# Optimization experiments

Hardware: AMD Instinct MI355X
Metric: run time of the kernel (lower is better)

The kernel has to match this reference:

```python
import jax, jax.numpy as jnp
import numpy as np

N = 20000      # num_atoms
C = 64         # num_features (channels)
I = 16         # num_irreps = (l_max+1)^2, l_max=3
K2, K1, K0 = 120, 8, 4  # CG basis sizes per correlation order


def setup_inputs() -> dict:
    key = jax.random.key(0)
    ks = jax.random.split(key, 7)
    return {
        "node_feats": jax.random.normal(ks[0], (N, C, I), jnp.float32),
        "U2": jax.random.normal(ks[1], (I, I, I, K2), jnp.float32),
        "U1": jax.random.normal(ks[2], (I, I, K1), jnp.float32),
        "U0": jax.random.normal(ks[3], (I, K0), jnp.float32),
        "w2": jax.random.normal(ks[4], (K2, C), jnp.float32),
        "w1": jax.random.normal(ks[5], (K1, C), jnp.float32),
        "w0": jax.random.normal(ks[6], (K0, C), jnp.float32),
    }


def reference(node_feats, U2, U1, U0, w2, w1, w0):
    # equation_main: '...ik,kc,bci -> bc...' with U2 [I,I,I,K2]
    # -> out [N, C, I, I]
    out = jnp.einsum('xyik,kc,nci->ncxy', U2, w2, node_feats)

    # corr = 1: weighting '...k,kc->c...' then contract 'bc...i,bci->bc...'
    c1 = jnp.einsum('xik,kc->cxi', U1, w1)          # [C, I, I]
    out = jnp.einsum('ncxi,nci->ncx', c1 + out, node_feats)  # [N, C, I]

    # corr = 0
    c0 = jnp.einsum('ik,kc->ci', U0, w0)            # [C, I]
    out = jnp.einsum('nci,nci->nc', c0 + out, node_feats)    # [N, C]
    return out
```

## Files before the change

kernel.cpp:

```cpp
#include <hip/hip_runtime.h>

#define NATOMS 20000
#define NCHAN  64
#define NIRR   16
#define K2 120
#define K1 8
#define K0 4

#define W1_BYTE_OFF 524288
#define W0_BYTE_OFF 557056

#define NT 10

typedef __attribute__((ext_vector_type(8))) short bf16x8;
typedef __attribute__((ext_vector_type(4))) float f32x4;
typedef __attribute__((ext_vector_type(4))) unsigned int u32x4;

__device__ inline short f2bf(float f) {
    union { float f; unsigned u; } v; v.f = f;
    unsigned r = v.u + 0x7FFF + ((v.u >> 16) & 1);
    return (short)(r >> 16);
}

__global__ __launch_bounds__(256) void precompute_kernel(
    const float* __restrict__ U2, const float* __restrict__ U1,
    const float* __restrict__ U0, const float* __restrict__ w2,
    const float* __restrict__ w1, const float* __restrict__ w0,
    void* __restrict__ wsv)
{
    short* W2bf = (short*)wsv;
    short* W1bf = (short*)((char*)wsv + W1_BYTE_OFF);
    float* W0f  = (float*)((char*)wsv + W0_BYTE_OFF);

    const int b = blockIdx.x;
    const int t = threadIdx.x;

    if (b < 256) {
        __shared__ __align__(16) float U2s[64][121];
        __shared__ __align__(16) float w2s[120][16];
        const int xyi0  = (b >> 2) * 64;
        const int cbase = (b & 3) * 16;

        for (int o = t; o < 64 * 120; o += 256) {
            int r = o / 120, k = o - r * 120;
            U2s[r][k] = U2[(size_t)xyi0 * 120 + o];
        }
        for (int o = t; o < 120 * 16; o += 256) {
            int k = o >> 4, cc = o & 15;
            w2s[k][cc] = w2[k * NCHAN + cbase + cc];
        }
        __syncthreads();

        const int r = t & 63;
        const int g = t >> 6;
        float acc0 = 0.f, acc1 = 0.f, acc2 = 0.f, acc3 = 0.f;
        #pragma unroll 8
        for (int k = 0; k < 120; ++k) {
            float u = U2s[r][k];
            float4 w = *(const float4*)&w2s[k][g * 4];
            acc0 += u * w.x; acc1 += u * w.y; acc2 += u * w.z; acc3 += u * w.w;
        }
        const int xyi = xyi0 + r;
        const int cA  = cbase + g * 4;
        W2bf[(size_t)(cA + 0) * 4096 + xyi] = f2bf(acc0);
        W2bf[(size_t)(cA + 1) * 4096 + xyi] = f2bf(acc1);
        W2bf[(size_t)(cA + 2) * 4096 + xyi] = f2bf(acc2);
        W2bf[(size_t)(cA + 3) * 4096 + xyi] = f2bf(acc3);
    } else {
        const int lb = b - 256;
        for (int o = t; o < 2048; o += 256) {
            int go = lb * 2048 + o;
            int c = go >> 8, xy = go & 255;
            const float* u = U1 + xy * K1;
            float acc = 0.f;
            #pragma unroll
            for (int k = 0; k < K1; ++k) acc += u[k] * w1[k * NCHAN + c];
            W1bf[c * 256 + xy] = f2bf(acc);
        }
        if (lb == 0) {
            for (int o = t; o < 1024; o += 256) {
                int c = o >> 4, x = o & 15;
                const float* u = U0 + x * K0;
                float acc = 0.f;
                #pragma unroll
                for (int k = 0; k < K0; ++k) acc += u[k] * w0[k * NCHAN + c];
                W0f[c * 16 + x] = acc;
            }
        }
    }
}

__device__ __forceinline__ void gload_lds16(const void* g, void* l) {
    __builtin_amdgcn_global_load_lds(
        (const __attribute__((address_space(1))) unsigned int*)g,
        (__attribute__((address_space(3))) unsigned int*)l, 16, 0, 0);
}

__device__ __forceinline__ float compute_tile(
    const bf16x8 (&aw)[16], float4 c0, int q,
    float4 va, float4 vb, float4 vc, float4 vd)
{
    float f0 = va.x, f1 = va.y, f2 = va.z, f3 = va.w;
    float f4 = vb.x, f5 = vb.y, f6 = vb.z, f7 = vb.w;
    float f8 = vc.x, f9 = vc.y, f10 = vc.z, f11 = vc.w;
    float f12 = vd.x, f13 = vd.y, f14 = vd.z, f15 = vd.w;

    unsigned pk0, pk1, pk2, pk3, pk4, pk5, pk6, pk7;
    asm("v_cvt_pk_bf16_f32 %0, %1, %2" : "=v"(pk0) : "v"(f0),  "v"(f1));
    asm("v_cvt_pk_bf16_f32 %0, %1, %2" : "=v"(pk1) : "v"(f2),  "v"(f3));
    asm("v_cvt_pk_bf16_f32 %0, %1, %2" : "=v"(pk2) : "v"(f4),  "v"(f5));
    asm("v_cvt_pk_bf16_f32 %0, %1, %2" : "=v"(pk3) : "v"(f6),  "v"(f7));
    asm("v_cvt_pk_bf16_f32 %0, %1, %2" : "=v"(pk4) : "v"(f8),  "v"(f9));
    asm("v_cvt_pk_bf16_f32 %0, %1, %2" : "=v"(pk5) : "v"(f10), "v"(f11));
    asm("v_cvt_pk_bf16_f32 %0, %1, %2" : "=v"(pk6) : "v"(f12), "v"(f13));
    asm("v_cvt_pk_bf16_f32 %0, %1, %2" : "=v"(pk7) : "v"(f14), "v"(f15));

    unsigned w0s = (q == 0) ? pk0 : (q == 1) ? pk4 : (q == 2) ? 0x00003f80u : 0u;
    unsigned w1s = (q == 0) ? pk1 : (q == 1) ? pk5 : 0u;
    unsigned w2s_ = (q == 0) ? pk2 : (q == 1) ? pk6 : 0u;
    unsigned w3s = (q == 0) ? pk3 : (q == 1) ? pk7 : 0u;
    u32x4 bu = {w0s, w1s, w2s_, w3s};
    bf16x8 bfr = __builtin_bit_cast(bf16x8, bu);

    const f32x4 z = {0.f, 0.f, 0.f, 0.f};
    f32x4 sy = z;
    f32x4 d0 = __builtin_amdgcn_mfma_f32_16x16x32_bf16(aw[0], bfr, z, 0, 0, 0);
    f32x4 d1 = __builtin_amdgcn_mfma_f32_16x16x32_bf16(aw[1], bfr, z, 0, 0, 0);
    f32x4 d2 = __builtin_amdgcn_mfma_f32_16x16x32_bf16(aw[2], bfr, z, 0, 0, 0);
    f32x4 d3 = __builtin_amdgcn_mfma_f32_16x16x32_bf16(aw[3], bfr, z, 0, 0, 0);
    sy += d0 * f0;  d0 = __builtin_amdgcn_mfma_f32_16x16x32_bf16(aw[4],  bfr, z, 0, 0, 0);
    sy += d1 * f1;  d1 = __builtin_amdgcn_mfma_f32_16x16x32_bf16(aw[5],  bfr, z, 0, 0, 0);
    sy += d2 * f2;  d2 = __builtin_amdgcn_mfma_f32_16x16x32_bf16(aw[6],  bfr, z, 0, 0, 0);
    sy += d3 * f3;  d3 = __builtin_amdgcn_mfma_f32_16x16x32_bf16(aw[7],  bfr, z, 0, 0, 0);
    sy += d0 * f4;  d0 = __builtin_amdgcn_mfma_f32_16x16x32_bf16(aw[8],  bfr, z, 0, 0, 0);
    sy += d1 * f5;  d1 = __builtin_amdgcn_mfma_f32_16x16x32_bf16(aw[9],  bfr, z, 0, 0, 0);
    sy += d2 * f6;  d2 = __builtin_amdgcn_mfma_f32_16x16x32_bf16(aw[10], bfr, z, 0, 0, 0);
    sy += d3 * f7;  d3 = __builtin_amdgcn_mfma_f32_16x16x32_bf16(aw[11], bfr, z, 0, 0, 0);
    sy += d0 * f8;  d0 = __builtin_amdgcn_mfma_f32_16x16x32_bf16(aw[12], bfr, z, 0, 0, 0);
    sy += d1 * f9;  d1 = __builtin_amdgcn_mfma_f32_16x16x32_bf16(aw[13], bfr, z, 0, 0, 0);
    sy += d2 * f10; d2 = __builtin_amdgcn_mfma_f32_16x16x32_bf16(aw[14], bfr, z, 0, 0, 0);
    sy += d3 * f11; d3 = __builtin_amdgcn_mfma_f32_16x16x32_bf16(aw[15], bfr, z, 0, 0, 0);
    sy += d0 * f12; sy += d1 * f13; sy += d2 * f14; sy += d3 * f15;

    float t0 = (q & 1) ? f4 : f0;   float u0 = (q & 1) ? f12 : f8;
    float fy0 = (q & 2) ? u0 : t0;
    float t1 = (q & 1) ? f5 : f1;   float u1 = (q & 1) ? f13 : f9;
    float fy1 = (q & 2) ? u1 : t1;
    float t2 = (q & 1) ? f6 : f2;   float u2 = (q & 1) ? f14 : f10;
    float fy2 = (q & 2) ? u2 : t2;
    float t3 = (q & 1) ? f7 : f3;   float u3 = (q & 1) ? f15 : f11;
    float fy3 = (q & 2) ? u3 : t3;

    float s = fy0 * (sy.x + c0.x);
    s = fmaf(fy1, sy.y + c0.y, s);
    s = fmaf(fy2, sy.z + c0.z, s);
    s = fmaf(fy3, sy.w + c0.w, s);
    s += __shfl_xor(s, 16);
    s += __shfl_xor(s, 32);
    return s;
}

__global__ __launch_bounds__(512, 3) void contract_kernel(
    const float* __restrict__ nf,
    const void* __restrict__ wsv,
    float* __restrict__ out)
{
    __shared__ __align__(16) float fs[2][2048];

    const short* W2g = (const short*)wsv;
    const short* W1g = (const short*)((const char*)wsv + W1_BYTE_OFF);
    const float* W0g = (const float*)((const char*)wsv + W0_BYTE_OFF);

    const int tid  = threadIdx.x;
    const int wave = tid >> 6;
    const int lane = tid & 63;
    const int m    = lane & 15;
    const int q    = lane >> 4;
    const int c    = blockIdx.x * 8 + wave;
    const int chunk = blockIdx.y;

    const int a_st = tid >> 5;
    const int soff = ((tid & 31) << 4) ^ ((a_st & 7) << 4);
    const char* sbase = (const char*)nf
        + ((size_t)(chunk * 160 + a_st) << 12)
        + ((size_t)blockIdx.x << 9)
        + soff;
    char* ldst0 = (char*)&fs[0][0] + (wave << 10);
    char* ldst1 = (char*)&fs[1][0] + (wave << 10);

    bf16x8 aw[16];
    #pragma unroll
    for (int j = 0; j < 16; ++j) {
        bf16x8 v = (bf16x8)0;
        if (q < 2) {
            v = *(const bf16x8*)(W2g + ((size_t)c << 12) + ((j * 16 + m) << 4) + (q << 3));
        } else if (q == 2) {
            v[0] = W1g[(c << 8) + (j << 4) + m];
        }
        aw[j] = v;
    }
    const float4 c0 = *(const float4*)(W0g + (c << 4) + (q << 2));

    const unsigned sw = (unsigned)((m & 7) << 4);
    const unsigned zb = (unsigned)(wave << 6);

    float outv[NT];

    gload_lds16(sbase, ldst0);

    #pragma unroll
    for (int T = 0; T < NT; ++T) {
        const int b = T & 1;
        if (T + 1 < NT)
            gload_lds16(sbase + (size_t)(T + 1) * 65536, b ? ldst0 : ldst1);
        if (T + 1 < NT) { asm volatile("s_waitcnt vmcnt(1)" ::: "memory"); }
        else            { asm volatile("s_waitcnt vmcnt(0)" ::: "memory"); }
        __builtin_amdgcn_s_barrier();

        const char* lrb = (const char*)&fs[b][0] + (m << 9);
        float4 va = *(const float4*)(lrb + ((zb +  0) ^ sw));
        float4 vb = *(const float4*)(lrb + ((zb + 16) ^ sw));
        float4 vc = *(const float4*)(lrb + ((zb + 32) ^ sw));
        float4 vd = *(const float4*)(lrb + ((zb + 48) ^ sw));

        outv[T] = compute_tile(aw, c0, q, va, vb, vc, vd);

        __builtin_amdgcn_s_barrier();
    }

    if (q == 0) {
        float* ob = out + ((size_t)(chunk * 160 + m)) * 64 + c;
        #pragma unroll
        for (int T = 0; T < NT; ++T)
            ob[(size_t)T * 1024] = outv[T];
    }
}

extern "C" void kernel_launch(void* const* d_in, const int* in_sizes, int n_in,
                              void* d_out, int out_size, void* d_ws, size_t ws_size,
                              hipStream_t stream)
{
    const float* nf = (const float*)d_in[0];
    const float* U2 = (const float*)d_in[1];
    const float* U1 = (const float*)d_in[2];
    const float* U0 = (const float*)d_in[3];
    const float* w2 = (const float*)d_in[4];
    const float* w1 = (const float*)d_in[5];
    const float* w0 = (const float*)d_in[6];
    float* out = (float*)d_out;

    precompute_kernel<<<264, 256, 0, stream>>>(U2, U1, U0, w2, w1, w0, d_ws);

    dim3 grid(8, 125);
    contract_kernel<<<grid, 512, 0, stream>>>(nf, d_ws, out);
}
```

Measured before the change: 176.2 us.

## Halve block size, deepen global-to-LDS prefetch to 3 stages, split accumulators

The contract kernel now uses 256-thread blocks of 4 channel-waves over a 16x125 grid, with smaller per-block LDS tiles and a new XOR swizzle. The double-buffered global-to-LDS load becomes a 4-slot ring with 3 loads in flight, using graded vmcnt waits. The aim is to hide memory latency better and raise block-level parallelism. The MFMA-result accumulation is split into two independent accumulators to shorten the dependency chain. Smaller blocks mean each nf row is fetched by twice as many blocks in narrower segments, and the deeper ring adds waits and a scheduling barrier.

```diff
diff --git a/kernel.cpp b/kernel.cpp
--- a/kernel.cpp
+++ b/kernel.cpp
@@ -11,6 +11,7 @@
 #define W0_BYTE_OFF 557056
 
 #define NT 10
+#define DEPTH 3
 
 typedef __attribute__((ext_vector_type(8))) short bf16x8;
 typedef __attribute__((ext_vector_type(4))) float f32x4;
@@ -123,24 +124,25 @@
     bf16x8 bfr = __builtin_bit_cast(bf16x8, bu);
 
     const f32x4 z = {0.f, 0.f, 0.f, 0.f};
-    f32x4 sy = z;
+    f32x4 syA = z, syB = z;
     f32x4 d0 = __builtin_amdgcn_mfma_f32_16x16x32_bf16(aw[0], bfr, z, 0, 0, 0);
     f32x4 d1 = __builtin_amdgcn_mfma_f32_16x16x32_bf16(aw[1], bfr, z, 0, 0, 0);
     f32x4 d2 = __builtin_amdgcn_mfma_f32_16x16x32_bf16(aw[2], bfr, z, 0, 0, 0);
     f32x4 d3 = __builtin_amdgcn_mfma_f32_16x16x32_bf16(aw[3], bfr, z, 0, 0, 0);
-    sy += d0 * f0;  d0 = __builtin_amdgcn_mfma_f32_16x16x32_bf16(aw[4],  bfr, z, 0, 0, 0);
-    sy += d1 * f1;  d1 = __builtin_amdgcn_mfma_f32_16x16x32_bf16(aw[5],  bfr, z, 0, 0, 0);
-    sy += d2 * f2;  d2 = __builtin_amdgcn_mfma_f32_16x16x32_bf16(aw[6],  bfr, z, 0, 0, 0);
-    sy += d3 * f3;  d3 = __builtin_amdgcn_mfma_f32_16x16x32_bf16(aw[7],  bfr, z, 0, 0, 0);
-    sy += d0 * f4;  d0 = __builtin_amdgcn_mfma_f32_16x16x32_bf16(aw[8],  bfr, z, 0, 0, 0);
-    sy += d1 * f5;  d1 = __builtin_amdgcn_mfma_f32_16x16x32_bf16(aw[9],  bfr, z, 0, 0, 0);
-    sy += d2 * f6;  d2 = __builtin_amdgcn_mfma_f32_16x16x32_bf16(aw[10], bfr, z, 0, 0, 0);
-    sy += d3 * f7;  d3 = __builtin_amdgcn_mfma_f32_16x16x32_bf16(aw[11], bfr, z, 0, 0, 0);
-    sy += d0 * f8;  d0 = __builtin_amdgcn_mfma_f32_16x16x32_bf16(aw[12], bfr, z, 0, 0, 0);
-    sy += d1 * f9;  d1 = __builtin_amdgcn_mfma_f32_16x16x32_bf16(aw[13], bfr, z, 0, 0, 0);
-    sy += d2 * f10; d2 = __builtin_amdgcn_mfma_f32_16x16x32_bf16(aw[14], bfr, z, 0, 0, 0);
-    sy += d3 * f11; d3 = __builtin_amdgcn_mfma_f32_16x16x32_bf16(aw[15], bfr, z, 0, 0, 0);
-    sy += d0 * f12; sy += d1 * f13; sy += d2 * f14; sy += d3 * f15;
+    syA += d0 * f0;  d0 = __builtin_amdgcn_mfma_f32_16x16x32_bf16(aw[4],  bfr, z, 0, 0, 0);
+    syB += d1 * f1;  d1 = __builtin_amdgcn_mfma_f32_16x16x32_bf16(aw[5],  bfr, z, 0, 0, 0);
+    syA += d2 * f2;  d2 = __builtin_amdgcn_mfma_f32_16x16x32_bf16(aw[6],  bfr, z, 0, 0, 0);
+    syB += d3 * f3;  d3 = __builtin_amdgcn_mfma_f32_16x16x32_bf16(aw[7],  bfr, z, 0, 0, 0);
+    syA += d0 * f4;  d0 = __builtin_amdgcn_mfma_f32_16x16x32_bf16(aw[8],  bfr, z, 0, 0, 0);
+    syB += d1 * f5;  d1 = __builtin_amdgcn_mfma_f32_16x16x32_bf16(aw[9],  bfr, z, 0, 0, 0);
+    syA += d2 * f6;  d2 = __builtin_amdgcn_mfma_f32_16x16x32_bf16(aw[10], bfr, z, 0, 0, 0);
+    syB += d3 * f7;  d3 = __builtin_amdgcn_mfma_f32_16x16x32_bf16(aw[11], bfr, z, 0, 0, 0);
+    syA += d0 * f8;  d0 = __builtin_amdgcn_mfma_f32_16x16x32_bf16(aw[12], bfr, z, 0, 0, 0);
+    syB += d1 * f9;  d1 = __builtin_amdgcn_mfma_f32_16x16x32_bf16(aw[13], bfr, z, 0, 0, 0);
+    syA += d2 * f10; d2 = __builtin_amdgcn_mfma_f32_16x16x32_bf16(aw[14], bfr, z, 0, 0, 0);
+    syB += d3 * f11; d3 = __builtin_amdgcn_mfma_f32_16x16x32_bf16(aw[15], bfr, z, 0, 0, 0);
+    syA += d0 * f12; syB += d1 * f13; syA += d2 * f14; syB += d3 * f15;
+    f32x4 sy = syA + syB;
 
     float t0 = (q & 1) ? f4 : f0;   float u0 = (q & 1) ? f12 : f8;
     float fy0 = (q & 2) ? u0 : t0;
@@ -160,12 +162,12 @@
     return s;
 }
 
-__global__ __launch_bounds__(512, 3) void contract_kernel(
+__global__ __launch_bounds__(256, 3) void contract_kernel(
     const float* __restrict__ nf,
     const void* __restrict__ wsv,
     float* __restrict__ out)
 {
-    __shared__ __align__(16) float fs[2][2048];
+    __shared__ __align__(16) float fs[4][1024];
 
     const short* W2g = (const short*)wsv;
     const short* W1g = (const short*)((const char*)wsv + W1_BYTE_OFF);
@@ -176,17 +178,17 @@
     const int lane = tid & 63;
     const int m    = lane & 15;
     const int q    = lane >> 4;
-    const int c    = blockIdx.x * 8 + wave;
+    const int c    = blockIdx.x * 4 + wave;
     const int chunk = blockIdx.y;
 
-    const int a_st = tid >> 5;
-    const int soff = ((tid & 31) << 4) ^ ((a_st & 7) << 4);
+    const int a_st = tid >> 4;
+    const int o_l  = (tid & 15) << 4;
+    const int o_g  = o_l ^ (a_st << 4);
     const char* sbase = (const char*)nf
         + ((size_t)(chunk * 160 + a_st) << 12)
-        + ((size_t)blockIdx.x << 9)
-        + soff;
-    char* ldst0 = (char*)&fs[0][0] + (wave << 10);
-    char* ldst1 = (char*)&fs[1][0] + (wave << 10);
+        + ((size_t)blockIdx.x << 8)
+        + o_g;
+    const unsigned ldw = (unsigned)(wave << 10);
 
     bf16x8 aw[16];
     #pragma unroll
@@ -201,23 +203,29 @@
     }
     const float4 c0 = *(const float4*)(W0g + (c << 4) + (q << 2));
 
-    const unsigned sw = (unsigned)((m & 7) << 4);
+    const unsigned sw = (unsigned)(m << 4);
     const unsigned zb = (unsigned)(wave << 6);
 
     float outv[NT];
 
-    gload_lds16(sbase, ldst0);
+    #pragma unroll
+    for (int t = 0; t < DEPTH; ++t)
+        gload_lds16(sbase + (size_t)t * 65536, (char*)&fs[t][0] + ldw);
 
     #pragma unroll
     for (int T = 0; T < NT; ++T) {
-        const int b = T & 1;
-        if (T + 1 < NT)
-            gload_lds16(sbase + (size_t)(T + 1) * 65536, b ? ldst0 : ldst1);
-        if (T + 1 < NT) { asm volatile("s_waitcnt vmcnt(1)" ::: "memory"); }
-        else            { asm volatile("s_waitcnt vmcnt(0)" ::: "memory"); }
+        if (T + DEPTH < NT)
+            gload_lds16(sbase + (size_t)(T + DEPTH) * 65536,
+                        (char*)&fs[(T + DEPTH) & 3][0] + ldw);
+        const int wcnt = (NT - 1 - T < DEPTH) ? (NT - 1 - T) : DEPTH;
+        if      (wcnt == 3) asm volatile("s_waitcnt vmcnt(3)" ::: "memory");
+        else if (wcnt == 2) asm volatile("s_waitcnt vmcnt(2)" ::: "memory");
+        else if (wcnt == 1) asm volatile("s_waitcnt vmcnt(1)" ::: "memory");
+        else                asm volatile("s_waitcnt vmcnt(0)" ::: "memory");
         __builtin_amdgcn_s_barrier();
-
-        const char* lrb = (const char*)&fs[b][0] + (m << 9);
+        __builtin_amdgcn_sched_barrier(0);
+
+        const char* lrb = (const char*)&fs[T & 3][0] + (m << 8);
         float4 va = *(const float4*)(lrb + ((zb +  0) ^ sw));
         float4 vb = *(const float4*)(lrb + ((zb + 16) ^ sw));
         float4 vc = *(const float4*)(lrb + ((zb + 32) ^ sw));
@@ -251,6 +259,6 @@
 
     precompute_kernel<<<264, 256, 0, stream>>>(U2, U1, U0, w2, w1, w0, d_ws);
 
-    dim3 grid(8, 125);
-    contract_kernel<<<grid, 512, 0, stream>>>(nf, d_ws, out);
-}
+    dim3 grid(16, 125);
+    contract_kernel<<<grid, 256, 0, stream>>>(nf, d_ws, out);
+}
```

After: 160.9 us. -8.7%, faster.
